# Performance work log

Measured on AMD Instinct MI355X. Metric: run time of the kernel, lower is better.

The kernel has to match this reference:

```python
import jax, jax.numpy as jnp
import numpy as np

VOCAB = 50257
EMB = 1024
HID = 1024
B, T = 8, 256


def setup_inputs() -> dict:
    key = jax.random.key(0)
    ks = jax.random.split(key, 6)
    s = 0.05  # small init scale for numerical sanity
    return {
        "x": jax.random.randint(ks[0], (B, T), 0, VOCAB, dtype=jnp.int64) if jax.config.jax_enable_x64 else jax.random.randint(ks[0], (B, T), 0, VOCAB, dtype=jnp.int32),
        "emb_W": jax.random.normal(ks[1], (VOCAB, EMB), dtype=jnp.float32) * s,
        "W_ih": jax.random.normal(ks[2], (4 * HID, EMB), dtype=jnp.float32) * s,
        "W_hh": jax.random.normal(ks[3], (4 * HID, HID), dtype=jnp.float32) * s,
        "b_ih": jax.random.normal(ks[4], (4 * HID,), dtype=jnp.float32) * s,
        "b_hh": jax.random.normal(ks[5], (4 * HID,), dtype=jnp.float32) * s,
        "dec_b": jnp.zeros((VOCAB,), dtype=jnp.float32),
    }


def _lstm(emb, W_ih, W_hh, b_ih, b_hh):
    # emb: [B, T, E]. Precompute input projections for all timesteps (one big GEMM).
    x_proj = jnp.einsum("bte,ge->btg", emb, W_ih) + (b_ih + b_hh)  # [B, T, 4H]
    h0 = jnp.zeros((emb.shape[0], HID), emb.dtype)
    c0 = jnp.zeros((emb.shape[0], HID), emb.dtype)

    def step(carry, xt):  # xt: [B, 4H]
        h, c = carry
        g = xt + h @ W_hh.T  # [B, 4H]
        i, f, gg, o = jnp.split(g, 4, axis=-1)  # PyTorch gate order i,f,g,o
        i = jax.nn.sigmoid(i)
        f = jax.nn.sigmoid(f)
        gg = jnp.tanh(gg)
        o = jax.nn.sigmoid(o)
        c_new = f * c + i * gg
        h_new = o * jnp.tanh(c_new)
        return (h_new, c_new), h_new

    (hT, cT), hs = jax.lax.scan(step, (h0, c0), jnp.swapaxes(x_proj, 0, 1))
    out = jnp.swapaxes(hs, 0, 1)  # [B, T, H], batch_first
    return out, (hT[None], cT[None])  # num_layers=1 leading dim


def reference(x, emb_W, W_ih, W_hh, b_ih, b_hh, dec_b):
    emb = emb_W[x]                                   # [B, T, E]
    out, hidden = _lstm(emb, W_ih, W_hh, b_ih, b_hh)  # [B, T, H]
    logits = jnp.einsum("bth,vh->btv", out, emb_W) + dec_b  # tied decoder
    logits = logits.reshape(-1, VOCAB)
    return jax.nn.log_softmax(logits, axis=1), hidden
```

## Files before the change

kernel.cpp:

```cpp
#include <hip/hip_runtime.h>

typedef float f32x4 __attribute__((ext_vector_type(4)));
typedef __bf16 bf16x8 __attribute__((ext_vector_type(8)));
typedef unsigned int u32x4 __attribute__((ext_vector_type(4)));
typedef unsigned short u16;
typedef unsigned int u32;

#define VOCAB 50257
#define KDIM 1024
#define MROWS 2048
#define TSEQ 256
#define NBLK 64
#define NHELP 192
#define NTILE 393
#define NT (NTILE * 2)
#define LOGN ((size_t)MROWS * VOCAB)

__device__ __forceinline__ u16 f2bf(float f) {
    u32 u = __builtin_bit_cast(u32, f);
    u = (u + 0x7FFFu + ((u >> 16) & 1u)) >> 16;
    return (u16)u;
}

__device__ __forceinline__ float sigm(float x) { return 1.0f / (1.0f + __expf(-x)); }

__device__ __forceinline__ u32 min4u(u32x4 v) {
    u32 a = v.x < v.y ? v.x : v.y;
    u32 b = v.z < v.w ? v.z : v.w;
    return a < b ? a : b;
}


__global__ void conv_bf16(const float4* __restrict__ in, ushort4* __restrict__ out, long n4) {
    long i = (long)blockIdx.x * blockDim.x + threadIdx.x;
    long stride = (long)gridDim.x * blockDim.x;
    for (; i < n4; i += stride) {
        float4 v = in[i];
        ushort4 o;
        o.x = f2bf(v.x); o.y = f2bf(v.y); o.z = f2bf(v.z); o.w = f2bf(v.w);
        out[i] = o;
    }
}

__global__ void bias_sum(const float* __restrict__ a, const float* __restrict__ b,
                         float* __restrict__ o) {
    int i = blockIdx.x * 256 + threadIdx.x;
    if (i < 4096) o[i] = a[i] + b[i];
}

__global__ __launch_bounds__(256) void gather_emb(const int* __restrict__ x,
                                                  const float* __restrict__ embW,
                                                  u16* __restrict__ out) {
    int m = blockIdx.x;
    int row = x[m];
    const float4* src = (const float4*)(embW + (size_t)row * KDIM);
    ushort4* dst = (ushort4*)(out + (size_t)m * KDIM);
    float4 v = src[threadIdx.x];
    ushort4 o;
    o.x = f2bf(v.x); o.y = f2bf(v.y); o.z = f2bf(v.z); o.w = f2bf(v.w);
    dst[threadIdx.x] = o;
}

__global__ void init_hseq(u32* __restrict__ hs) {
    int i = blockIdx.x * 256 + threadIdx.x;
    if (i < 257 * 4096) hs[i] = (i < 4096) ? 0x00010001u : 0u;
}


#define BM 128
#define BN 128
#define BK 64

__device__ __forceinline__ void gl_lds16(const u16* g, const u16* l) {
    __builtin_amdgcn_global_load_lds(
        (const __attribute__((address_space(1))) u32*)g,
        (__attribute__((address_space(3))) u32*)l, 16, 0, 0);
}

__global__ __launch_bounds__(256, 2)
void gemm_bt(const u16* __restrict__ A, const u16* __restrict__ Bm,
             const float* __restrict__ bias, float* __restrict__ C,
             int N, int Nb, int K, int ldc)
{
    __shared__ __align__(16) u16 As[BM * BK];
    __shared__ __align__(16) u16 Bs[BN * BK];
    const int tid  = threadIdx.x;
    const int lane = tid & 63;
    const int wid  = tid >> 6;

    const int gx  = gridDim.x;
    const int nwg = gx * gridDim.y;
    const int lin = blockIdx.y * gx + blockIdx.x;
    const int qq = nwg >> 3, rr = nwg & 7;
    const int xcd = lin & 7, idx = lin >> 3;
    const int neu = (xcd < rr) ? (xcd * (qq + 1) + idx)
                               : (rr * (qq + 1) + (xcd - rr) * qq + idx);
    const int bm = neu % gx;
    const int bn = neu / gx;

    const int wr = wid >> 1, wc = wid & 1;

    const u16* gA[4]; const u16* gB[4];
    const u16* ldsA[4]; const u16* ldsB[4];
#pragma unroll
    for (int r = 0; r < 4; ++r) {
        int L = r * 256 + tid;
        int row = L >> 3, ps = L & 7;
        int ls = ps ^ (row & 7);
        gA[r] = A + (size_t)(bm * BM + row) * K + ls * 8;
        int brow = bn * BN + row; brow = brow < Nb ? brow : Nb - 1;
        gB[r] = Bm + (size_t)brow * K + ls * 8;
        ldsA[r] = As + (r * 256 + wid * 64) * 8;
        ldsB[r] = Bs + (r * 256 + wid * 64) * 8;
    }

    const int lrow = lane & 15, ksl = lane >> 4;
    int aoff[4][2], boff[4][2];
#pragma unroll
    for (int i = 0; i < 4; ++i)
#pragma unroll
        for (int ks = 0; ks < 2; ++ks) {
            int ar = wr * 64 + i * 16 + lrow;
            aoff[i][ks] = ar * BK + (((ks * 4 + ksl) ^ (ar & 7)) * 8);
            int br = wc * 64 + i * 16 + lrow;
            boff[i][ks] = br * BK + (((ks * 4 + ksl) ^ (br & 7)) * 8);
        }

    f32x4 acc[4][4] = {};
    for (int kt = 0; kt < K; kt += BK) {
#pragma unroll
        for (int r = 0; r < 4; ++r) gl_lds16(gA[r] + kt, ldsA[r]);
#pragma unroll
        for (int r = 0; r < 4; ++r) gl_lds16(gB[r] + kt, ldsB[r]);
        __syncthreads();
        bf16x8 af[4][2], bfb[4][2];
#pragma unroll
        for (int i = 0; i < 4; ++i)
#pragma unroll
            for (int ks = 0; ks < 2; ++ks) {
                af[i][ks]  = *(const bf16x8*)(As + aoff[i][ks]);
                bfb[i][ks] = *(const bf16x8*)(Bs + boff[i][ks]);
            }
#pragma unroll
        for (int ks = 0; ks < 2; ++ks)
#pragma unroll
            for (int mi = 0; mi < 4; ++mi)
#pragma unroll
                for (int ni = 0; ni < 4; ++ni)
                    acc[mi][ni] = __builtin_amdgcn_mfma_f32_16x16x32_bf16(
                        af[mi][ks], bfb[ni][ks], acc[mi][ni], 0, 0, 0);
        __syncthreads();
    }

    const int crl = lane >> 4, ccl = lane & 15;
    const int row0 = bm * BM + wr * 64, col0 = bn * BN + wc * 64;
#pragma unroll
    for (int ni = 0; ni < 4; ++ni) {
        int col = col0 + ni * 16 + ccl;
        if (col < N) {
            float bv = bias[col];
#pragma unroll
            for (int mi = 0; mi < 4; ++mi) {
                int row = row0 + mi * 16 + crl * 4;
                float* cp = C + (size_t)row * ldc + col;
#pragma unroll
                for (int r = 0; r < 4; ++r)
                    cp[(size_t)r * ldc] = acc[mi][ni][r] + bv;
            }
        }
    }
}


__global__ __launch_bounds__(256, 2)
void gemm_dec(const u16* __restrict__ A, const u16* __restrict__ Bm,
              const float* __restrict__ bias, u16* __restrict__ Cb,
              float* __restrict__ pmax, float* __restrict__ psum)
{
    const int N = VOCAB, Nb = VOCAB, K = KDIM;
    __shared__ __align__(16) u16 As[BM * BK];
    __shared__ __align__(16) u16 Bs[BN * BK];
    const int tid  = threadIdx.x;
    const int lane = tid & 63;
    const int wid  = tid >> 6;

    const int gx  = gridDim.x;
    const int nwg = gx * gridDim.y;
    const int lin = blockIdx.y * gx + blockIdx.x;
    const int qq = nwg >> 3, rr = nwg & 7;
    const int xcd = lin & 7, idx = lin >> 3;
    const int neu = (xcd < rr) ? (xcd * (qq + 1) + idx)
                               : (rr * (qq + 1) + (xcd - rr) * qq + idx);
    const int bm = neu % gx;
    const int bn = neu / gx;

    const int wr = wid >> 1, wc = wid & 1;

    const u16* gA[4]; const u16* gB[4];
    const u16* ldsA[4]; const u16* ldsB[4];
#pragma unroll
    for (int r = 0; r < 4; ++r) {
        int L = r * 256 + tid;
        int row = L >> 3, ps = L & 7;
        int ls = ps ^ (row & 7);
        gA[r] = A + (size_t)(bm * BM + row) * K + ls * 8;
        int brow = bn * BN + row; brow = brow < Nb ? brow : Nb - 1;
        gB[r] = Bm + (size_t)brow * K + ls * 8;
        ldsA[r] = As + (r * 256 + wid * 64) * 8;
        ldsB[r] = Bs + (r * 256 + wid * 64) * 8;
    }

    const int lrow = lane & 15, ksl = lane >> 4;
    int aoff[4][2], boff[4][2];
#pragma unroll
    for (int i = 0; i < 4; ++i)
#pragma unroll
        for (int ks = 0; ks < 2; ++ks) {
            int ar = wr * 64 + i * 16 + lrow;
            aoff[i][ks] = ar * BK + (((ks * 4 + ksl) ^ (ar & 7)) * 8);
            int br = wc * 64 + i * 16 + lrow;
            boff[i][ks] = br * BK + (((ks * 4 + ksl) ^ (br & 7)) * 8);
        }

    f32x4 acc[4][4] = {};
    for (int kt = 0; kt < K; kt += BK) {
#pragma unroll
        for (int r = 0; r < 4; ++r) gl_lds16(gA[r] + kt, ldsA[r]);
#pragma unroll
        for (int r = 0; r < 4; ++r) gl_lds16(gB[r] + kt, ldsB[r]);
        __syncthreads();
        bf16x8 af[4][2], bfb[4][2];
#pragma unroll
        for (int i = 0; i < 4; ++i)
#pragma unroll
            for (int ks = 0; ks < 2; ++ks) {
                af[i][ks]  = *(const bf16x8*)(As + aoff[i][ks]);
                bfb[i][ks] = *(const bf16x8*)(Bs + boff[i][ks]);
            }
#pragma unroll
        for (int ks = 0; ks < 2; ++ks)
#pragma unroll
            for (int mi = 0; mi < 4; ++mi)
#pragma unroll
                for (int ni = 0; ni < 4; ++ni)
                    acc[mi][ni] = __builtin_amdgcn_mfma_f32_16x16x32_bf16(
                        af[mi][ks], bfb[ni][ks], acc[mi][ni], 0, 0, 0);
        __syncthreads();
    }

    const int crl = lane >> 4, ccl = lane & 15;
    const int row0 = bm * BM + wr * 64, col0 = bn * BN + wc * 64;
    float bve[4]; bool vld[4];
#pragma unroll
    for (int ni = 0; ni < 4; ++ni) {
        int col = col0 + ni * 16 + ccl;
        vld[ni] = col < N;
        bve[ni] = vld[ni] ? bias[col] : 0.f;
    }
#pragma unroll
    for (int ni = 0; ni < 4; ++ni) {
        if (vld[ni]) {
            int col = col0 + ni * 16 + ccl;
#pragma unroll
            for (int mi = 0; mi < 4; ++mi) {
                int row = row0 + mi * 16 + crl * 4;
                u16* cp = Cb + (size_t)row * (VOCAB * 2) + col;
#pragma unroll
                for (int r = 0; r < 4; ++r)
                    cp[(size_t)r * (VOCAB * 2)] = f2bf(acc[mi][ni][r] + bve[ni]);
            }
        }
    }
#pragma unroll
    for (int mi = 0; mi < 4; ++mi)
#pragma unroll
        for (int r = 0; r < 4; ++r) {
            int row = row0 + mi * 16 + crl * 4 + r;
            float v0 = vld[0] ? acc[mi][0][r] + bve[0] : -3.0e38f;
            float v1 = vld[1] ? acc[mi][1][r] + bve[1] : -3.0e38f;
            float v2 = vld[2] ? acc[mi][2][r] + bve[2] : -3.0e38f;
            float v3 = vld[3] ? acc[mi][3][r] + bve[3] : -3.0e38f;
            float rmax = fmaxf(fmaxf(v0, v1), fmaxf(v2, v3));
#pragma unroll
            for (int m2 = 1; m2 < 16; m2 <<= 1) rmax = fmaxf(rmax, __shfl_xor(rmax, m2));
            float rs = __expf(v0 - rmax) + __expf(v1 - rmax) +
                       __expf(v2 - rmax) + __expf(v3 - rmax);
#pragma unroll
            for (int m2 = 1; m2 < 16; m2 <<= 1) rs += __shfl_xor(rs, m2);
            if (ccl == 0) {
                pmax[(size_t)row * NT + bn * 2 + wc] = rmax;
                psum[(size_t)row * NT + bn * 2 + wc] = rs;
            }
        }
}


__global__ __launch_bounds__(256, 1)
void lstm_persist(const u16* __restrict__ Whh,
                  const float* __restrict__ xproj,
                  u16* __restrict__ hseq,
                  u16* __restrict__ hall,
                  float* __restrict__ outTail,
                  const float4* __restrict__ embW,
                  ushort4* __restrict__ embW_bf)
{
    const int tid = threadIdx.x;
    const int bid = blockIdx.x;

    if (bid >= NBLK) {
        long i = (long)(bid - NBLK) * 256 + tid;
        const long n4 = (long)VOCAB * KDIM / 4;
        const long stride = (long)NHELP * 256;
        for (; i < n4; i += stride) {
            float4 v = embW[i];
            ushort4 o;
            o.x = f2bf(v.x); o.y = f2bf(v.y); o.z = f2bf(v.z); o.w = f2bf(v.w);
            embW_bf[i] = o;
        }
        return;
    }

    const int lane = tid & 63;
    const int wq   = tid >> 6;
    const int lrow = lane & 15, ksl = lane >> 4;
    const int colbase = bid * 16;

    bf16x8 Bf[32];
    {
        const u16* bp = Whh + (size_t)(wq * 1024 + colbase + lrow) * KDIM + ksl * 8;
#pragma unroll
        for (int kk = 0; kk < 32; ++kk)
            asm volatile("global_load_dwordx4 %0, %1, off"
                         : "=v"(Bf[kk]) : "v"(bp + kk * 32));
        asm volatile("s_waitcnt vmcnt(0)" ::: "memory");
        __builtin_amdgcn_sched_barrier(0);
    }

    __shared__ float S[4][8][16];
    __shared__ __align__(16) u16 hstage[2][16384];

    for (int i = tid; i < 2 * 64 * 8; i += 256) {
        int buf = i >> 9, rem = i & 511;
        int j = rem >> 3, rowoff = rem & 7;
        u32x4 z = {0, 0, 0, 0};
        *(u32x4*)(&hstage[buf][j * 256 + 128 + rowoff * 16]) = z;
        *(u32x4*)(&hstage[buf][j * 256 + 128 + rowoff * 16 + 8]) = z;
    }

    const bool upd = tid < 128;
    const int b8 = tid >> 4, c16 = tid & 15;
    float creg = 0.f;
    float xp0 = 0.f, xp1 = 0.f, xp2 = 0.f, xp3 = 0.f;
    size_t xbase = 0;
    if (upd) {
        xbase = (size_t)b8 * TSEQ * 4096 + colbase + c16;
        xp0 = xproj[xbase];          xp1 = xproj[xbase + 1024];
        xp2 = xproj[xbase + 2048];   xp3 = xproj[xbase + 3072];
    }

    const int pj = tid >> 2, pr = (tid & 3) * 2;
    const int sw = (pj & 7) << 3;
    int widx[4];
#pragma unroll
    for (int k = 0; k < 4; ++k)
        widx[k] = pj * 256 + ((pr * 16 + k * 8) ^ sw);

    int aro[4];
#pragma unroll
    for (int i = 0; i < 4; ++i) {
        int swr = ((2 * i + (ksl >> 1)) & 7) << 3;
        aro[i] = (ksl >> 1) * 256 + ((lrow * 16 + (ksl & 1) * 8) ^ swr);
    }

    for (int t = 0; t < TSEQ; ++t) {
        const u32* src = (const u32*)hseq + (size_t)t * 4096 + pj * 64 + pr * 8;
        u32x4 P0, P1, P2, P3;
        for (;;) {
            asm volatile("global_load_dwordx4 %0, %1, off sc0 sc1" : "=v"(P0) : "v"(src));
            asm volatile("global_load_dwordx4 %0, %1, off sc0 sc1" : "=v"(P1) : "v"(src + 4));
            asm volatile("global_load_dwordx4 %0, %1, off sc0 sc1" : "=v"(P2) : "v"(src + 8));
            asm volatile("global_load_dwordx4 %0, %1, off sc0 sc1" : "=v"(P3) : "v"(src + 12));
            asm volatile("s_waitcnt vmcnt(0)" ::: "memory");
            __builtin_amdgcn_sched_barrier(0);
            u32 a = min4u(P0), b = min4u(P1), c = min4u(P2), d = min4u(P3);
            u32 mn = (a < b ? a : b); u32 mn2 = (c < d ? c : d);
            if ((mn < mn2 ? mn : mn2) != 0u) break;
        }
        {
            u16* hb = &hstage[t & 1][0];
            *(u32x4*)(hb + widx[0]) = P0;
            *(u32x4*)(hb + widx[1]) = P1;
            *(u32x4*)(hb + widx[2]) = P2;
            *(u32x4*)(hb + widx[3]) = P3;
        }
        __syncthreads();

        const u16* sb = &hstage[t & 1][0];
        f32x4 ac0 = {}, ac1 = {}, ac2 = {}, ac3 = {};
#pragma unroll
        for (int g = 0; g < 8; ++g) {
            bf16x8 a0 = *(const bf16x8*)(sb + g * 2048 + 0 * 512 + aro[0]);
            bf16x8 a1 = *(const bf16x8*)(sb + g * 2048 + 1 * 512 + aro[1]);
            bf16x8 a2 = *(const bf16x8*)(sb + g * 2048 + 2 * 512 + aro[2]);
            bf16x8 a3 = *(const bf16x8*)(sb + g * 2048 + 3 * 512 + aro[3]);
            ac0 = __builtin_amdgcn_mfma_f32_16x16x32_bf16(a0, Bf[g * 4 + 0], ac0, 0, 0, 0);
            ac1 = __builtin_amdgcn_mfma_f32_16x16x32_bf16(a1, Bf[g * 4 + 1], ac1, 0, 0, 0);
            ac2 = __builtin_amdgcn_mfma_f32_16x16x32_bf16(a2, Bf[g * 4 + 2], ac2, 0, 0, 0);
            ac3 = __builtin_amdgcn_mfma_f32_16x16x32_bf16(a3, Bf[g * 4 + 3], ac3, 0, 0, 0);
        }
        if (ksl < 2) {
#pragma unroll
            for (int r = 0; r < 4; ++r)
                S[wq][ksl * 4 + r][lrow] = ac0[r] + ac1[r] + ac2[r] + ac3[r];
        }
        __syncthreads();

        if (upd) {
            float gi = S[0][b8][c16] + xp0;
            float gf = S[1][b8][c16] + xp1;
            float gg = S[2][b8][c16] + xp2;
            float go = S[3][b8][c16] + xp3;
            float iv = sigm(gi), fv = sigm(gf), ov = sigm(go);
            float gv = tanhf(gg);
            creg = fv * creg + iv * gv;
            float hv = ov * tanhf(creg);
            u16 hbx = f2bf(hv) | 1;
            int w0 = (int)hbx;
            int w1 = __shfl_down(w0, 1);
            if (!(c16 & 1)) {
                u32 w = (u32)(u16)w0 | ((u32)(u16)w1 << 16);
                u32* dst = (u32*)hseq + (size_t)(t + 1) * 4096 + bid * 64 + b8 * 8 + (c16 >> 1);
                __hip_atomic_store(dst, w, __ATOMIC_RELAXED, __HIP_MEMORY_SCOPE_AGENT);
            }
            hall[((size_t)b8 * TSEQ + t) * KDIM + colbase + c16] = hbx;
            if (t == TSEQ - 1) {
                outTail[b8 * KDIM + colbase + c16] = hv;
                outTail[8192 + b8 * KDIM + colbase + c16] = creg;
            }
            int tn = (t + 1 < TSEQ) ? t + 1 : t;
            size_t xb = xbase + (size_t)tn * 4096;
            xp0 = xproj[xb];        xp1 = xproj[xb + 1024];
            xp2 = xproj[xb + 2048]; xp3 = xproj[xb + 3072];
        }
    }
}


__global__ __launch_bounds__(256)
void merge_lse(const float* __restrict__ pmax, const float* __restrict__ psum,
               float* __restrict__ lse) {
    const int m = blockIdx.x;
    const int tid = threadIdx.x;
    __shared__ float smx[4], ssm[4];
    float mx = -3.0e38f, s = 0.f;
    for (int i = tid; i < NT; i += 256) {
        float pm = pmax[(size_t)m * NT + i];
        float ps = psum[(size_t)m * NT + i];
        if (pm > mx) { s *= __expf(mx - pm); mx = pm; }
        s += ps * __expf(pm - mx);
    }
#pragma unroll
    for (int off = 32; off > 0; off >>= 1) {
        float om = __shfl_xor(mx, off), os = __shfl_xor(s, off);
        float nm = fmaxf(mx, om);
        s = s * __expf(mx - nm) + os * __expf(om - nm);
        mx = nm;
    }
    if ((tid & 63) == 0) { smx[tid >> 6] = mx; ssm[tid >> 6] = s; }
    __syncthreads();
    if (tid == 0) {
        float M = fmaxf(fmaxf(smx[0], smx[1]), fmaxf(smx[2], smx[3]));
        float S4 = ssm[0] * __expf(smx[0] - M) + ssm[1] * __expf(smx[1] - M) +
                   ssm[2] * __expf(smx[2] - M) + ssm[3] * __expf(smx[3] - M);
        lse[m] = M + __logf(S4);
    }
}

__global__ __launch_bounds__(256)
void final_sub(float* __restrict__ out, const float* __restrict__ lse) {
    const int m = blockIdx.x;
    const float L = lse[m];
    const u32* srcw = (const u32*)out + (size_t)m * VOCAB;
    float* dst = out + (size_t)m * VOCAB;
    const int tid = threadIdx.x;
    const int NCH = (VOCAB + 2047) / 2048;
    for (int c = NCH - 1; c >= 0; --c) {
        int e0 = c * 2048 + tid * 8;
        int w0i = e0 >> 1;
        u32 w0 = srcw[w0i], w1 = srcw[w0i + 1], w2 = srcw[w0i + 2], w3 = srcw[w0i + 3];
        __syncthreads();
        float f[8];
        f[0] = __builtin_bit_cast(float, (w0 & 0xFFFFu) << 16) - L;
        f[1] = __builtin_bit_cast(float, w0 & 0xFFFF0000u) - L;
        f[2] = __builtin_bit_cast(float, (w1 & 0xFFFFu) << 16) - L;
        f[3] = __builtin_bit_cast(float, w1 & 0xFFFF0000u) - L;
        f[4] = __builtin_bit_cast(float, (w2 & 0xFFFFu) << 16) - L;
        f[5] = __builtin_bit_cast(float, w2 & 0xFFFF0000u) - L;
        f[6] = __builtin_bit_cast(float, (w3 & 0xFFFFu) << 16) - L;
        f[7] = __builtin_bit_cast(float, w3 & 0xFFFF0000u) - L;
        if (e0 + 8 <= VOCAB) {
#pragma unroll
            for (int k = 0; k < 8; ++k) dst[e0 + k] = f[k];
        } else {
#pragma unroll
            for (int k = 0; k < 8; ++k) if (e0 + k < VOCAB) dst[e0 + k] = f[k];
        }
    }
}


extern "C" void kernel_launch(void* const* d_in, const int* in_sizes, int n_in,
                              void* d_out, int out_size, void* d_ws, size_t ws_size,
                              hipStream_t stream)
{
    const int*   x    = (const int*)d_in[0];
    const float* embW = (const float*)d_in[1];
    const float* Wih  = (const float*)d_in[2];
    const float* Whh  = (const float*)d_in[3];
    const float* bih  = (const float*)d_in[4];
    const float* bhh  = (const float*)d_in[5];
    const float* decb = (const float*)d_in[6];
    float* out = (float*)d_out;

    char* p = (char*)d_ws;
    auto carve = [&](size_t bytes) {
        char* q = p;
        p += (bytes + 255) & ~(size_t)255;
        return q;
    };
    u16*   embW_bf = (u16*)carve((size_t)VOCAB * KDIM * 2);
    u16*   Wih_bf  = (u16*)carve((size_t)4096 * KDIM * 2);
    u16*   Whh_bf  = (u16*)carve((size_t)4096 * KDIM * 2);
    u16*   emb_bf  = (u16*)carve((size_t)MROWS * KDIM * 2);
    float* xproj   = (float*)carve((size_t)MROWS * 4096 * 4);
    u16*   hall_bf = (u16*)carve((size_t)MROWS * KDIM * 2);
    u16*   hseq    = (u16*)carve((size_t)(TSEQ + 1) * 4096 * 4);
    float* pmax    = (float*)carve((size_t)MROWS * NT * 4);
    float* psum    = (float*)carve((size_t)MROWS * NT * 4);
    float* lse     = (float*)carve((size_t)MROWS * 4);
    float* bsum    = (float*)carve((size_t)4096 * 4);

    init_hseq<<<(257 * 4096 + 255) / 256, 256, 0, stream>>>((u32*)hseq);

    conv_bf16<<<1024, 256, 0, stream>>>((const float4*)Wih, (ushort4*)Wih_bf,
                                        (long)4096 * KDIM / 4);
    conv_bf16<<<1024, 256, 0, stream>>>((const float4*)Whh, (ushort4*)Whh_bf,
                                        (long)4096 * KDIM / 4);
    bias_sum<<<16, 256, 0, stream>>>(bih, bhh, bsum);
    gather_emb<<<MROWS, 256, 0, stream>>>(x, embW, emb_bf);

    {
        dim3 g(MROWS / BM, 4096 / BN);
        gemm_bt<<<g, 256, 0, stream>>>(emb_bf, Wih_bf, bsum, xproj, 4096, 4096, KDIM, 4096);
    }

    lstm_persist<<<NBLK + NHELP, 256, 0, stream>>>(Whh_bf, xproj, hseq, hall_bf,
                                                   out + LOGN,
                                                   (const float4*)embW,
                                                   (ushort4*)embW_bf);

    {
        dim3 g(MROWS / BM, NTILE);
        gemm_dec<<<g, 256, 0, stream>>>(hall_bf, embW_bf, decb, (u16*)out, pmax, psum);
    }

    merge_lse<<<MROWS, 256, 0, stream>>>(pmax, psum, lse);
    final_sub<<<MROWS, 256, 0, stream>>>(out, lse);
}
```

Baseline: 1.217 ms.

## Place persistent LSTM blocks on one XCD and use cheaper coherent polling

Each block reads its XCD id and takes a per-XCD ticket. The first XCD to collect 64 blocks becomes the leader, and only its blocks run the recurrent LSTM, so the per-step h exchange stays inside one die's L2. Every other block converts the embedding table to bf16. Polling first uses L2-coherent (sc0) loads and falls back to system-coherent loads after 8 tries. Each h store is written twice, once to the local L2 and once system-coherent. The launch becomes cooperative with 512 blocks at 2 blocks per CU to guarantee co-residency. The cost is extra atomics and memsets, and it relies on the hardware mapping blocks to XCDs.

```diff
diff --git a/kernel.cpp b/kernel.cpp
--- a/kernel.cpp
+++ b/kernel.cpp
@@ -11,7 +11,7 @@
 #define MROWS 2048
 #define TSEQ 256
 #define NBLK 64
-#define NHELP 192
+#define NTOT 512
 #define NTILE 393
 #define NT (NTILE * 2)
 #define LOGN ((size_t)MROWS * VOCAB)
@@ -295,22 +295,54 @@
 }
 
 
-__global__ __launch_bounds__(256, 1)
+__global__ __launch_bounds__(256, 2)
 void lstm_persist(const u16* __restrict__ Whh,
                   const float* __restrict__ xproj,
                   u16* __restrict__ hseq,
                   u16* __restrict__ hall,
                   float* __restrict__ outTail,
                   const float4* __restrict__ embW,
-                  ushort4* __restrict__ embW_bf)
+                  ushort4* __restrict__ embW_bf,
+                  u32* __restrict__ cnt,
+                  u32* __restrict__ leader,
+                  u32* __restrict__ helpc)
 {
     const int tid = threadIdx.x;
-    const int bid = blockIdx.x;
-
-    if (bid >= NBLK) {
-        long i = (long)(bid - NBLK) * 256 + tid;
+    __shared__ u32 roleS;
+
+    if (tid == 0) {
+        u32 xcd;
+        asm volatile("s_getreg_b32 %0, hwreg(HW_REG_XCC_ID)" : "=s"(xcd));
+        xcd &= 7u;
+        u32 ticket = __hip_atomic_fetch_add(&cnt[xcd * 32], 1u,
+                                            __ATOMIC_RELAXED, __HIP_MEMORY_SCOPE_AGENT);
+        u32 slot = 0xFFFFFFFFu;
+        if (ticket < NBLK) {
+            if (ticket == NBLK - 1) {
+                u32 expect = 0xFFFFFFFFu;
+                __hip_atomic_compare_exchange_strong(leader, &expect, xcd,
+                    __ATOMIC_RELAXED, __ATOMIC_RELAXED, __HIP_MEMORY_SCOPE_AGENT);
+            }
+            u32 L;
+            while ((L = __hip_atomic_load(leader, __ATOMIC_RELAXED,
+                                          __HIP_MEMORY_SCOPE_AGENT)) == 0xFFFFFFFFu)
+                __builtin_amdgcn_s_sleep(2);
+            if (L == xcd) slot = ticket;
+        }
+        roleS = slot;
+    }
+    __syncthreads();
+    const u32 slot = roleS;
+
+    if (slot == 0xFFFFFFFFu) {
+        __shared__ u32 hidxS;
+        if (tid == 0)
+            hidxS = __hip_atomic_fetch_add(helpc, 1u,
+                                           __ATOMIC_RELAXED, __HIP_MEMORY_SCOPE_AGENT);
+        __syncthreads();
+        long i = (long)hidxS * 256 + tid;
         const long n4 = (long)VOCAB * KDIM / 4;
-        const long stride = (long)NHELP * 256;
+        const long stride = (long)(NTOT - NBLK) * 256;
         for (; i < n4; i += stride) {
             float4 v = embW[i];
             ushort4 o;
@@ -323,7 +355,7 @@
     const int lane = tid & 63;
     const int wq   = tid >> 6;
     const int lrow = lane & 15, ksl = lane >> 4;
-    const int colbase = bid * 16;
+    const int colbase = slot * 16;
 
     bf16x8 Bf[32];
     {
@@ -375,11 +407,18 @@
     for (int t = 0; t < TSEQ; ++t) {
         const u32* src = (const u32*)hseq + (size_t)t * 4096 + pj * 64 + pr * 8;
         u32x4 P0, P1, P2, P3;
-        for (;;) {
-            asm volatile("global_load_dwordx4 %0, %1, off sc0 sc1" : "=v"(P0) : "v"(src));
-            asm volatile("global_load_dwordx4 %0, %1, off sc0 sc1" : "=v"(P1) : "v"(src + 4));
-            asm volatile("global_load_dwordx4 %0, %1, off sc0 sc1" : "=v"(P2) : "v"(src + 8));
-            asm volatile("global_load_dwordx4 %0, %1, off sc0 sc1" : "=v"(P3) : "v"(src + 12));
+        for (int tries = 0;; ++tries) {
+            if (tries < 8) {
+                asm volatile("global_load_dwordx4 %0, %1, off sc0" : "=v"(P0) : "v"(src));
+                asm volatile("global_load_dwordx4 %0, %1, off sc0" : "=v"(P1) : "v"(src + 4));
+                asm volatile("global_load_dwordx4 %0, %1, off sc0" : "=v"(P2) : "v"(src + 8));
+                asm volatile("global_load_dwordx4 %0, %1, off sc0" : "=v"(P3) : "v"(src + 12));
+            } else {
+                asm volatile("global_load_dwordx4 %0, %1, off sc0 sc1" : "=v"(P0) : "v"(src));
+                asm volatile("global_load_dwordx4 %0, %1, off sc0 sc1" : "=v"(P1) : "v"(src + 4));
+                asm volatile("global_load_dwordx4 %0, %1, off sc0 sc1" : "=v"(P2) : "v"(src + 8));
+                asm volatile("global_load_dwordx4 %0, %1, off sc0 sc1" : "=v"(P3) : "v"(src + 12));
+            }
             asm volatile("s_waitcnt vmcnt(0)" ::: "memory");
             __builtin_amdgcn_sched_barrier(0);
             u32 a = min4u(P0), b = min4u(P1), c = min4u(P2), d = min4u(P3);
@@ -429,8 +468,10 @@
             int w1 = __shfl_down(w0, 1);
             if (!(c16 & 1)) {
                 u32 w = (u32)(u16)w0 | ((u32)(u16)w1 << 16);
-                u32* dst = (u32*)hseq + (size_t)(t + 1) * 4096 + bid * 64 + b8 * 8 + (c16 >> 1);
-                __hip_atomic_store(dst, w, __ATOMIC_RELAXED, __HIP_MEMORY_SCOPE_AGENT);
+                u32* dst = (u32*)hseq + (size_t)(t + 1) * 4096 + slot * 64 + b8 * 8 + (c16 >> 1);
+                asm volatile("global_store_dword %0, %1, off\n\t"
+                             "global_store_dword %0, %1, off sc0 sc1"
+                             :: "v"(dst), "v"(w) : "memory");
             }
             hall[((size_t)b8 * TSEQ + t) * KDIM + colbase + c16] = hbx;
             if (t == TSEQ - 1) {
@@ -539,6 +580,13 @@
     float* psum    = (float*)carve((size_t)MROWS * NT * 4);
     float* lse     = (float*)carve((size_t)MROWS * 4);
     float* bsum    = (float*)carve((size_t)4096 * 4);
+    u32*   cnt     = (u32*)carve(8 * 32 * 4);
+    u32*   leader  = (u32*)carve(256);
+    u32*   helpc   = (u32*)carve(256);
+
+    hipMemsetAsync(cnt, 0, 8 * 32 * 4, stream);
+    hipMemsetAsync(leader, 0xFF, 4, stream);
+    hipMemsetAsync(helpc, 0, 4, stream);
 
     init_hseq<<<(257 * 4096 + 255) / 256, 256, 0, stream>>>((u32*)hseq);
 
@@ -554,10 +602,21 @@
         gemm_bt<<<g, 256, 0, stream>>>(emb_bf, Wih_bf, bsum, xproj, 4096, 4096, KDIM, 4096);
     }
 
-    lstm_persist<<<NBLK + NHELP, 256, 0, stream>>>(Whh_bf, xproj, hseq, hall_bf,
-                                                   out + LOGN,
-                                                   (const float4*)embW,
-                                                   (ushort4*)embW_bf);
+    {
+        const u16* a0 = Whh_bf; const float* a1 = xproj; u16* a2 = hseq;
+        u16* a3 = hall_bf; float* a4 = out + LOGN;
+        const float4* a5 = (const float4*)embW; ushort4* a6 = (ushort4*)embW_bf;
+        u32* a7 = cnt; u32* a8 = leader; u32* a9 = helpc;
+        void* args[] = { &a0, &a1, &a2, &a3, &a4, &a5, &a6, &a7, &a8, &a9 };
+        hipError_t e = hipLaunchCooperativeKernel((const void*)lstm_persist,
+                                                  dim3(NTOT), dim3(256),
+                                                  args, 0, stream);
+        if (e != hipSuccess) {
+            lstm_persist<<<NTOT, 256, 0, stream>>>(Whh_bf, xproj, hseq, hall_bf,
+                                                   out + LOGN, (const float4*)embW,
+                                                   (ushort4*)embW_bf, cnt, leader, helpc);
+        }
+    }
 
     {
         dim3 g(MROWS / BM, NTILE);
```

New measurement: 2.041 ms. 67.8% more time.

## Interleave W_hh gate rows so LSTM cell update runs in-register without LDS barrier

Applied to the files above, without the earlier changes.

Reorders the W_hh rows loaded per lane so each MFMA output quad holds the i,f,g,o gates of one hidden column. Gates are then gathered with lane shuffles and the cell update is done directly in registers, removing the shared-memory gate buffer and one __syncthreads per timestep on the serial recurrent critical path. The trade-off is that fewer lanes (a quarter of those in the first half of each wave) do the nonlinearities, each handling four batch rows, and the per-step xproj loads become more scattered.

```diff
diff --git a/kernel.cpp b/kernel.cpp
--- a/kernel.cpp
+++ b/kernel.cpp
@@ -321,13 +321,15 @@
     }
 
     const int lane = tid & 63;
-    const int wq   = tid >> 6;
+    const int w    = tid >> 6;
     const int lrow = lane & 15, ksl = lane >> 4;
     const int colbase = bid * 16;
+    const int q  = lrow & 3;
+    const int cc = lrow >> 2;
 
     bf16x8 Bf[32];
     {
-        const u16* bp = Whh + (size_t)(wq * 1024 + colbase + lrow) * KDIM + ksl * 8;
+        const u16* bp = Whh + (size_t)(q * 1024 + colbase + w * 4 + cc) * KDIM + ksl * 8;
 #pragma unroll
         for (int kk = 0; kk < 32; ++kk)
             asm volatile("global_load_dwordx4 %0, %1, off"
@@ -336,7 +338,6 @@
         __builtin_amdgcn_sched_barrier(0);
     }
 
-    __shared__ float S[4][8][16];
     __shared__ __align__(16) u16 hstage[2][16384];
 
     for (int i = tid; i < 2 * 64 * 8; i += 256) {
@@ -347,15 +348,17 @@
         *(u32x4*)(&hstage[buf][j * 256 + 128 + rowoff * 16 + 8]) = z;
     }
 
-    const bool upd = tid < 128;
-    const int b8 = tid >> 4, c16 = tid & 15;
-    float creg = 0.f;
-    float xp0 = 0.f, xp1 = 0.f, xp2 = 0.f, xp3 = 0.f;
-    size_t xbase = 0;
-    if (upd) {
-        xbase = (size_t)b8 * TSEQ * 4096 + colbase + c16;
-        xp0 = xproj[xbase];          xp1 = xproj[xbase + 1024];
-        xp2 = xproj[xbase + 2048];   xp3 = xproj[xbase + 3072];
+    const int mycol = colbase + w * 4 + cc;
+    const bool updl = (q == 0) && (ksl < 2);
+    f32x4 creg = {};
+    f32x4 xg0 = {}, xg1 = {}, xg2 = {}, xg3 = {};
+    if (updl) {
+#pragma unroll
+        for (int r = 0; r < 4; ++r) {
+            size_t xb = ((size_t)(ksl * 4 + r) * TSEQ) * 4096 + mycol;
+            xg0[r] = xproj[xb];        xg1[r] = xproj[xb + 1024];
+            xg2[r] = xproj[xb + 2048]; xg3[r] = xproj[xb + 3072];
+        }
     }
 
     const int pj = tid >> 2, pr = (tid & 3) * 2;
@@ -387,11 +390,11 @@
             if ((mn < mn2 ? mn : mn2) != 0u) break;
         }
         {
-            u16* hb = &hstage[t & 1][0];
-            *(u32x4*)(hb + widx[0]) = P0;
-            *(u32x4*)(hb + widx[1]) = P1;
-            *(u32x4*)(hb + widx[2]) = P2;
-            *(u32x4*)(hb + widx[3]) = P3;
+            u16* hb2 = &hstage[t & 1][0];
+            *(u32x4*)(hb2 + widx[0]) = P0;
+            *(u32x4*)(hb2 + widx[1]) = P1;
+            *(u32x4*)(hb2 + widx[2]) = P2;
+            *(u32x4*)(hb2 + widx[3]) = P3;
         }
         __syncthreads();
 
@@ -408,39 +411,65 @@
             ac2 = __builtin_amdgcn_mfma_f32_16x16x32_bf16(a2, Bf[g * 4 + 2], ac2, 0, 0, 0);
             ac3 = __builtin_amdgcn_mfma_f32_16x16x32_bf16(a3, Bf[g * 4 + 3], ac3, 0, 0, 0);
         }
-        if (ksl < 2) {
-#pragma unroll
-            for (int r = 0; r < 4; ++r)
-                S[wq][ksl * 4 + r][lrow] = ac0[r] + ac1[r] + ac2[r] + ac3[r];
-        }
-        __syncthreads();
-
-        if (upd) {
-            float gi = S[0][b8][c16] + xp0;
-            float gf = S[1][b8][c16] + xp1;
-            float gg = S[2][b8][c16] + xp2;
-            float go = S[3][b8][c16] + xp3;
-            float iv = sigm(gi), fv = sigm(gf), ov = sigm(go);
-            float gv = tanhf(gg);
-            creg = fv * creg + iv * gv;
-            float hv = ov * tanhf(creg);
-            u16 hbx = f2bf(hv) | 1;
-            int w0 = (int)hbx;
-            int w1 = __shfl_down(w0, 1);
-            if (!(c16 & 1)) {
-                u32 w = (u32)(u16)w0 | ((u32)(u16)w1 << 16);
-                u32* dst = (u32*)hseq + (size_t)(t + 1) * 4096 + bid * 64 + b8 * 8 + (c16 >> 1);
-                __hip_atomic_store(dst, w, __ATOMIC_RELAXED, __HIP_MEMORY_SCOPE_AGENT);
-            }
-            hall[((size_t)b8 * TSEQ + t) * KDIM + colbase + c16] = hbx;
+
+        f32x4 D = ac0 + ac1 + ac2 + ac3;
+        float s1x[4], s2x[4], s3x[4];
+#pragma unroll
+        for (int r = 0; r < 4; ++r) {
+            s1x[r] = __shfl_down(D[r], 1);
+            s2x[r] = __shfl_down(D[r], 2);
+            s3x[r] = __shfl_down(D[r], 3);
+        }
+
+        float hv[4] = {0.f, 0.f, 0.f, 0.f};
+        int hb[4] = {0, 0, 0, 0};
+        if (updl) {
+#pragma unroll
+            for (int r = 0; r < 4; ++r) {
+                float gi = D[r]   + xg0[r];
+                float gf = s1x[r] + xg1[r];
+                float gg = s2x[r] + xg2[r];
+                float go = s3x[r] + xg3[r];
+                float iv = sigm(gi), fv = sigm(gf), ov = sigm(go);
+                float gv = tanhf(gg);
+                creg[r] = fv * creg[r] + iv * gv;
+                hv[r] = ov * tanhf(creg[r]);
+                hb[r] = (int)(f2bf(hv[r]) | 1);
+            }
+        }
+        int nb0 = __shfl_down(hb[0], 4);
+        int nb1 = __shfl_down(hb[1], 4);
+        int nb2 = __shfl_down(hb[2], 4);
+        int nb3 = __shfl_down(hb[3], 4);
+
+        if (updl) {
+            if (!(cc & 1)) {
+                int nbv[4] = {nb0, nb1, nb2, nb3};
+#pragma unroll
+                for (int r = 0; r < 4; ++r) {
+                    u32 wp = (u32)(u16)hb[r] | ((u32)(u16)nbv[r] << 16);
+                    u32* dst = (u32*)hseq + (size_t)(t + 1) * 4096 + bid * 64
+                               + (ksl * 4 + r) * 8 + ((w * 4 + cc) >> 1);
+                    __hip_atomic_store(dst, wp, __ATOMIC_RELAXED, __HIP_MEMORY_SCOPE_AGENT);
+                    u32* hd = (u32*)hall
+                              + (((size_t)(ksl * 4 + r) * TSEQ + t) * KDIM + mycol) / 2;
+                    *hd = wp;
+                }
+            }
             if (t == TSEQ - 1) {
-                outTail[b8 * KDIM + colbase + c16] = hv;
-                outTail[8192 + b8 * KDIM + colbase + c16] = creg;
+#pragma unroll
+                for (int r = 0; r < 4; ++r) {
+                    outTail[(ksl * 4 + r) * KDIM + mycol] = hv[r];
+                    outTail[8192 + (ksl * 4 + r) * KDIM + mycol] = creg[r];
+                }
             }
             int tn = (t + 1 < TSEQ) ? t + 1 : t;
-            size_t xb = xbase + (size_t)tn * 4096;
-            xp0 = xproj[xb];        xp1 = xproj[xb + 1024];
-            xp2 = xproj[xb + 2048]; xp3 = xproj[xb + 3072];
+#pragma unroll
+            for (int r = 0; r < 4; ++r) {
+                size_t xb = ((size_t)(ksl * 4 + r) * TSEQ + tn) * 4096 + mycol;
+                xg0[r] = xproj[xb];        xg1[r] = xproj[xb + 1024];
+                xg2[r] = xproj[xb + 2048]; xg3[r] = xproj[xb + 3072];
+            }
         }
     }
 }
```

Result: slower. 1.887 ms (+55.1%).

## Fuse decoder GEMM into persistent LSTM kernel with dynamic tile queue

Applied to the files above, without the earlier changes.

Removes the separate decoder GEMM launch. Helper blocks, after converting the embedding to bf16, and the LSTM blocks, after finishing the recurrence, pull decoder tiles from an atomic work queue. Each tile spin-waits until its 128 rows of hidden states are flagged ready in hall, so decoding overlaps the serial recurrence. The cost is that the 64 recurrence blocks share the GPU with concurrent GEMM work, which may slow the latency-critical LSTM chain. It also adds polling, coherent loads of the A operand through registers instead of direct-to-LDS loads, and only 256 resident blocks with one block per CU.

```diff
diff --git a/kernel.cpp b/kernel.cpp
--- a/kernel.cpp
+++ b/kernel.cpp
@@ -3,6 +3,7 @@
 typedef float f32x4 __attribute__((ext_vector_type(4)));
 typedef __bf16 bf16x8 __attribute__((ext_vector_type(8)));
 typedef unsigned int u32x4 __attribute__((ext_vector_type(4)));
+typedef unsigned int u32x2 __attribute__((ext_vector_type(2)));
 typedef unsigned short u16;
 typedef unsigned int u32;
 
@@ -14,6 +15,7 @@
 #define NHELP 192
 #define NTILE 393
 #define NT (NTILE * 2)
+#define NTILES_TOT (16 * NTILE)
 #define LOGN ((size_t)MROWS * VOCAB)
 
 __device__ __forceinline__ u16 f2bf(float f) {
@@ -66,6 +68,11 @@
     if (i < 257 * 4096) hs[i] = (i < 4096) ? 0x00010001u : 0u;
 }
 
+__global__ void zero_hall(u32* __restrict__ h) {
+    int i = blockIdx.x * 256 + threadIdx.x;
+    if (i < MROWS * (KDIM / 2)) h[i] = 0u;
+}
+
 
 #define BM 128
 #define BN 128
@@ -172,45 +179,29 @@
 }
 
 
-__global__ __launch_bounds__(256, 2)
-void gemm_dec(const u16* __restrict__ A, const u16* __restrict__ Bm,
-              const float* __restrict__ bias, u16* __restrict__ Cb,
-              float* __restrict__ pmax, float* __restrict__ psum)
+__device__ __forceinline__ void dec_tile(
+    const u16* __restrict__ A, const u16* __restrict__ Bm,
+    const float* __restrict__ bias, u16* __restrict__ Cb,
+    float* __restrict__ pmax, float* __restrict__ psum,
+    u16* As, u16* Bs, int bm, int bn, int tid)
 {
-    const int N = VOCAB, Nb = VOCAB, K = KDIM;
-    __shared__ __align__(16) u16 As[BM * BK];
-    __shared__ __align__(16) u16 Bs[BN * BK];
-    const int tid  = threadIdx.x;
     const int lane = tid & 63;
     const int wid  = tid >> 6;
-
-    const int gx  = gridDim.x;
-    const int nwg = gx * gridDim.y;
-    const int lin = blockIdx.y * gx + blockIdx.x;
-    const int qq = nwg >> 3, rr = nwg & 7;
-    const int xcd = lin & 7, idx = lin >> 3;
-    const int neu = (xcd < rr) ? (xcd * (qq + 1) + idx)
-                               : (rr * (qq + 1) + (xcd - rr) * qq + idx);
-    const int bm = neu % gx;
-    const int bn = neu / gx;
-
     const int wr = wid >> 1, wc = wid & 1;
-
-    const u16* gA[4]; const u16* gB[4];
-    const u16* ldsA[4]; const u16* ldsB[4];
+    const int lrow = lane & 15, ksl = lane >> 4;
+
+    const u16* gB[4]; const u16* ldsB[4];
+    const u16* gA[4]; u16* wA[4];
 #pragma unroll
     for (int r = 0; r < 4; ++r) {
         int L = r * 256 + tid;
         int row = L >> 3, ps = L & 7;
-        int ls = ps ^ (row & 7);
-        gA[r] = A + (size_t)(bm * BM + row) * K + ls * 8;
-        int brow = bn * BN + row; brow = brow < Nb ? brow : Nb - 1;
-        gB[r] = Bm + (size_t)brow * K + ls * 8;
-        ldsA[r] = As + (r * 256 + wid * 64) * 8;
+        int brow = bn * BN + row; brow = brow < VOCAB ? brow : VOCAB - 1;
+        gB[r] = Bm + (size_t)brow * KDIM + (ps ^ (row & 7)) * 8;
         ldsB[r] = Bs + (r * 256 + wid * 64) * 8;
-    }
-
-    const int lrow = lane & 15, ksl = lane >> 4;
+        gA[r] = A + (size_t)(bm * BM + row) * KDIM + ps * 8;
+        wA[r] = As + row * BK + ((ps ^ (row & 7)) * 8);
+    }
     int aoff[4][2], boff[4][2];
 #pragma unroll
     for (int i = 0; i < 4; ++i)
@@ -223,11 +214,18 @@
         }
 
     f32x4 acc[4][4] = {};
-    for (int kt = 0; kt < K; kt += BK) {
-#pragma unroll
-        for (int r = 0; r < 4; ++r) gl_lds16(gA[r] + kt, ldsA[r]);
+    for (int kt = 0; kt < KDIM; kt += BK) {
+        bf16x8 Ar[4];
 #pragma unroll
         for (int r = 0; r < 4; ++r) gl_lds16(gB[r] + kt, ldsB[r]);
+#pragma unroll
+        for (int r = 0; r < 4; ++r)
+            asm volatile("global_load_dwordx4 %0, %1, off sc0 sc1"
+                         : "=v"(Ar[r]) : "v"(gA[r] + kt));
+        asm volatile("s_waitcnt vmcnt(0)" ::: "memory");
+        __builtin_amdgcn_sched_barrier(0);
+#pragma unroll
+        for (int r = 0; r < 4; ++r) *(bf16x8*)wA[r] = Ar[r];
         __syncthreads();
         bf16x8 af[4][2], bfb[4][2];
 #pragma unroll
@@ -254,7 +252,7 @@
 #pragma unroll
     for (int ni = 0; ni < 4; ++ni) {
         int col = col0 + ni * 16 + ccl;
-        vld[ni] = col < N;
+        vld[ni] = col < VOCAB;
         bve[ni] = vld[ni] ? bias[col] : 0.f;
     }
 #pragma unroll
@@ -302,10 +300,19 @@
                   u16* __restrict__ hall,
                   float* __restrict__ outTail,
                   const float4* __restrict__ embW,
-                  ushort4* __restrict__ embW_bf)
+                  u16* __restrict__ embW_bf,
+                  const float* __restrict__ decb,
+                  u16* __restrict__ Cb,
+                  float* __restrict__ pmax, float* __restrict__ psum,
+                  u32* __restrict__ qcnt,
+                  u32* __restrict__ convc)
 {
     const int tid = threadIdx.x;
     const int bid = blockIdx.x;
+
+    __shared__ float S[4][8][16];
+    __shared__ __align__(16) u16 hstage[2][16384];
+    __shared__ int tileS;
 
     if (bid >= NBLK) {
         long i = (long)(bid - NBLK) * 256 + tid;
@@ -315,133 +322,172 @@
             float4 v = embW[i];
             ushort4 o;
             o.x = f2bf(v.x); o.y = f2bf(v.y); o.z = f2bf(v.z); o.w = f2bf(v.w);
-            embW_bf[i] = o;
-        }
-        return;
-    }
-
-    const int lane = tid & 63;
-    const int wq   = tid >> 6;
-    const int lrow = lane & 15, ksl = lane >> 4;
-    const int colbase = bid * 16;
-
-    bf16x8 Bf[32];
-    {
-        const u16* bp = Whh + (size_t)(wq * 1024 + colbase + lrow) * KDIM + ksl * 8;
-#pragma unroll
-        for (int kk = 0; kk < 32; ++kk)
-            asm volatile("global_load_dwordx4 %0, %1, off"
-                         : "=v"(Bf[kk]) : "v"(bp + kk * 32));
+            asm volatile("global_store_dwordx2 %0, %1, off sc0 sc1"
+                         :: "v"((ushort4*)embW_bf + i), "v"(o) : "memory");
+        }
         asm volatile("s_waitcnt vmcnt(0)" ::: "memory");
-        __builtin_amdgcn_sched_barrier(0);
-    }
-
-    __shared__ float S[4][8][16];
-    __shared__ __align__(16) u16 hstage[2][16384];
-
-    for (int i = tid; i < 2 * 64 * 8; i += 256) {
-        int buf = i >> 9, rem = i & 511;
-        int j = rem >> 3, rowoff = rem & 7;
-        u32x4 z = {0, 0, 0, 0};
-        *(u32x4*)(&hstage[buf][j * 256 + 128 + rowoff * 16]) = z;
-        *(u32x4*)(&hstage[buf][j * 256 + 128 + rowoff * 16 + 8]) = z;
-    }
-
-    const bool upd = tid < 128;
-    const int b8 = tid >> 4, c16 = tid & 15;
-    float creg = 0.f;
-    float xp0 = 0.f, xp1 = 0.f, xp2 = 0.f, xp3 = 0.f;
-    size_t xbase = 0;
-    if (upd) {
-        xbase = (size_t)b8 * TSEQ * 4096 + colbase + c16;
-        xp0 = xproj[xbase];          xp1 = xproj[xbase + 1024];
-        xp2 = xproj[xbase + 2048];   xp3 = xproj[xbase + 3072];
-    }
-
-    const int pj = tid >> 2, pr = (tid & 3) * 2;
-    const int sw = (pj & 7) << 3;
-    int widx[4];
-#pragma unroll
-    for (int k = 0; k < 4; ++k)
-        widx[k] = pj * 256 + ((pr * 16 + k * 8) ^ sw);
-
-    int aro[4];
-#pragma unroll
-    for (int i = 0; i < 4; ++i) {
-        int swr = ((2 * i + (ksl >> 1)) & 7) << 3;
-        aro[i] = (ksl >> 1) * 256 + ((lrow * 16 + (ksl & 1) * 8) ^ swr);
-    }
-
-    for (int t = 0; t < TSEQ; ++t) {
-        const u32* src = (const u32*)hseq + (size_t)t * 4096 + pj * 64 + pr * 8;
-        u32x4 P0, P1, P2, P3;
-        for (;;) {
-            asm volatile("global_load_dwordx4 %0, %1, off sc0 sc1" : "=v"(P0) : "v"(src));
-            asm volatile("global_load_dwordx4 %0, %1, off sc0 sc1" : "=v"(P1) : "v"(src + 4));
-            asm volatile("global_load_dwordx4 %0, %1, off sc0 sc1" : "=v"(P2) : "v"(src + 8));
-            asm volatile("global_load_dwordx4 %0, %1, off sc0 sc1" : "=v"(P3) : "v"(src + 12));
+        if (tid == 0) {
+            __hip_atomic_fetch_add(convc, 1u, __ATOMIC_RELAXED, __HIP_MEMORY_SCOPE_AGENT);
+            while (__hip_atomic_load(convc, __ATOMIC_RELAXED,
+                                     __HIP_MEMORY_SCOPE_AGENT) < (u32)NHELP)
+                __builtin_amdgcn_s_sleep(4);
+        }
+        __syncthreads();
+    } else {
+        const int lane = tid & 63;
+        const int wq   = tid >> 6;
+        const int lrow = lane & 15, ksl = lane >> 4;
+        const int colbase = bid * 16;
+
+        bf16x8 Bf[32];
+        {
+            const u16* bp = Whh + (size_t)(wq * 1024 + colbase + lrow) * KDIM + ksl * 8;
+#pragma unroll
+            for (int kk = 0; kk < 32; ++kk)
+                asm volatile("global_load_dwordx4 %0, %1, off"
+                             : "=v"(Bf[kk]) : "v"(bp + kk * 32));
             asm volatile("s_waitcnt vmcnt(0)" ::: "memory");
             __builtin_amdgcn_sched_barrier(0);
-            u32 a = min4u(P0), b = min4u(P1), c = min4u(P2), d = min4u(P3);
-            u32 mn = (a < b ? a : b); u32 mn2 = (c < d ? c : d);
-            if ((mn < mn2 ? mn : mn2) != 0u) break;
-        }
-        {
-            u16* hb = &hstage[t & 1][0];
-            *(u32x4*)(hb + widx[0]) = P0;
-            *(u32x4*)(hb + widx[1]) = P1;
-            *(u32x4*)(hb + widx[2]) = P2;
-            *(u32x4*)(hb + widx[3]) = P3;
-        }
-        __syncthreads();
-
-        const u16* sb = &hstage[t & 1][0];
-        f32x4 ac0 = {}, ac1 = {}, ac2 = {}, ac3 = {};
-#pragma unroll
-        for (int g = 0; g < 8; ++g) {
-            bf16x8 a0 = *(const bf16x8*)(sb + g * 2048 + 0 * 512 + aro[0]);
-            bf16x8 a1 = *(const bf16x8*)(sb + g * 2048 + 1 * 512 + aro[1]);
-            bf16x8 a2 = *(const bf16x8*)(sb + g * 2048 + 2 * 512 + aro[2]);
-            bf16x8 a3 = *(const bf16x8*)(sb + g * 2048 + 3 * 512 + aro[3]);
-            ac0 = __builtin_amdgcn_mfma_f32_16x16x32_bf16(a0, Bf[g * 4 + 0], ac0, 0, 0, 0);
-            ac1 = __builtin_amdgcn_mfma_f32_16x16x32_bf16(a1, Bf[g * 4 + 1], ac1, 0, 0, 0);
-            ac2 = __builtin_amdgcn_mfma_f32_16x16x32_bf16(a2, Bf[g * 4 + 2], ac2, 0, 0, 0);
-            ac3 = __builtin_amdgcn_mfma_f32_16x16x32_bf16(a3, Bf[g * 4 + 3], ac3, 0, 0, 0);
-        }
-        if (ksl < 2) {
-#pragma unroll
-            for (int r = 0; r < 4; ++r)
-                S[wq][ksl * 4 + r][lrow] = ac0[r] + ac1[r] + ac2[r] + ac3[r];
-        }
-        __syncthreads();
-
+        }
+
+        for (int i = tid; i < 2 * 64 * 8; i += 256) {
+            int buf = i >> 9, rem = i & 511;
+            int j = rem >> 3, rowoff = rem & 7;
+            u32x4 z = {0, 0, 0, 0};
+            *(u32x4*)(&hstage[buf][j * 256 + 128 + rowoff * 16]) = z;
+            *(u32x4*)(&hstage[buf][j * 256 + 128 + rowoff * 16 + 8]) = z;
+        }
+
+        const bool upd = tid < 128;
+        const int b8 = tid >> 4, c16 = tid & 15;
+        float creg = 0.f;
+        float xp0 = 0.f, xp1 = 0.f, xp2 = 0.f, xp3 = 0.f;
+        size_t xbase = 0;
         if (upd) {
-            float gi = S[0][b8][c16] + xp0;
-            float gf = S[1][b8][c16] + xp1;
-            float gg = S[2][b8][c16] + xp2;
-            float go = S[3][b8][c16] + xp3;
-            float iv = sigm(gi), fv = sigm(gf), ov = sigm(go);
-            float gv = tanhf(gg);
-            creg = fv * creg + iv * gv;
-            float hv = ov * tanhf(creg);
-            u16 hbx = f2bf(hv) | 1;
-            int w0 = (int)hbx;
-            int w1 = __shfl_down(w0, 1);
-            if (!(c16 & 1)) {
-                u32 w = (u32)(u16)w0 | ((u32)(u16)w1 << 16);
-                u32* dst = (u32*)hseq + (size_t)(t + 1) * 4096 + bid * 64 + b8 * 8 + (c16 >> 1);
-                __hip_atomic_store(dst, w, __ATOMIC_RELAXED, __HIP_MEMORY_SCOPE_AGENT);
-            }
-            hall[((size_t)b8 * TSEQ + t) * KDIM + colbase + c16] = hbx;
-            if (t == TSEQ - 1) {
-                outTail[b8 * KDIM + colbase + c16] = hv;
-                outTail[8192 + b8 * KDIM + colbase + c16] = creg;
-            }
-            int tn = (t + 1 < TSEQ) ? t + 1 : t;
-            size_t xb = xbase + (size_t)tn * 4096;
-            xp0 = xproj[xb];        xp1 = xproj[xb + 1024];
-            xp2 = xproj[xb + 2048]; xp3 = xproj[xb + 3072];
-        }
+            xbase = (size_t)b8 * TSEQ * 4096 + colbase + c16;
+            xp0 = xproj[xbase];          xp1 = xproj[xbase + 1024];
+            xp2 = xproj[xbase + 2048];   xp3 = xproj[xbase + 3072];
+        }
+
+        const int pj = tid >> 2, pr = (tid & 3) * 2;
+        const int sw = (pj & 7) << 3;
+        int widx[4];
+#pragma unroll
+        for (int k = 0; k < 4; ++k)
+            widx[k] = pj * 256 + ((pr * 16 + k * 8) ^ sw);
+
+        int aro[4];
+#pragma unroll
+        for (int i = 0; i < 4; ++i) {
+            int swr = ((2 * i + (ksl >> 1)) & 7) << 3;
+            aro[i] = (ksl >> 1) * 256 + ((lrow * 16 + (ksl & 1) * 8) ^ swr);
+        }
+
+        for (int t = 0; t < TSEQ; ++t) {
+            const u32* src = (const u32*)hseq + (size_t)t * 4096 + pj * 64 + pr * 8;
+            u32x4 P0, P1, P2, P3;
+            for (;;) {
+                asm volatile("global_load_dwordx4 %0, %1, off sc0 sc1" : "=v"(P0) : "v"(src));
+                asm volatile("global_load_dwordx4 %0, %1, off sc0 sc1" : "=v"(P1) : "v"(src + 4));
+                asm volatile("global_load_dwordx4 %0, %1, off sc0 sc1" : "=v"(P2) : "v"(src + 8));
+                asm volatile("global_load_dwordx4 %0, %1, off sc0 sc1" : "=v"(P3) : "v"(src + 12));
+                asm volatile("s_waitcnt vmcnt(0)" ::: "memory");
+                __builtin_amdgcn_sched_barrier(0);
+                u32 a = min4u(P0), b = min4u(P1), c = min4u(P2), d = min4u(P3);
+                u32 mn = (a < b ? a : b); u32 mn2 = (c < d ? c : d);
+                if ((mn < mn2 ? mn : mn2) != 0u) break;
+            }
+            {
+                u16* hb2 = &hstage[t & 1][0];
+                *(u32x4*)(hb2 + widx[0]) = P0;
+                *(u32x4*)(hb2 + widx[1]) = P1;
+                *(u32x4*)(hb2 + widx[2]) = P2;
+                *(u32x4*)(hb2 + widx[3]) = P3;
+            }
+            __syncthreads();
+
+            const u16* sb = &hstage[t & 1][0];
+            f32x4 ac0 = {}, ac1 = {}, ac2 = {}, ac3 = {};
+#pragma unroll
+            for (int g = 0; g < 8; ++g) {
+                bf16x8 a0 = *(const bf16x8*)(sb + g * 2048 + 0 * 512 + aro[0]);
+                bf16x8 a1 = *(const bf16x8*)(sb + g * 2048 + 1 * 512 + aro[1]);
+                bf16x8 a2 = *(const bf16x8*)(sb + g * 2048 + 2 * 512 + aro[2]);
+                bf16x8 a3 = *(const bf16x8*)(sb + g * 2048 + 3 * 512 + aro[3]);
+                ac0 = __builtin_amdgcn_mfma_f32_16x16x32_bf16(a0, Bf[g * 4 + 0], ac0, 0, 0, 0);
+                ac1 = __builtin_amdgcn_mfma_f32_16x16x32_bf16(a1, Bf[g * 4 + 1], ac1, 0, 0, 0);
+                ac2 = __builtin_amdgcn_mfma_f32_16x16x32_bf16(a2, Bf[g * 4 + 2], ac2, 0, 0, 0);
+                ac3 = __builtin_amdgcn_mfma_f32_16x16x32_bf16(a3, Bf[g * 4 + 3], ac3, 0, 0, 0);
+            }
+            if (ksl < 2) {
+#pragma unroll
+                for (int r = 0; r < 4; ++r)
+                    S[wq][ksl * 4 + r][lrow] = ac0[r] + ac1[r] + ac2[r] + ac3[r];
+            }
+            __syncthreads();
+
+            if (upd) {
+                float gi = S[0][b8][c16] + xp0;
+                float gf = S[1][b8][c16] + xp1;
+                float gg = S[2][b8][c16] + xp2;
+                float go = S[3][b8][c16] + xp3;
+                float iv = sigm(gi), fv = sigm(gf), ov = sigm(go);
+                float gv = tanhf(gg);
+                creg = fv * creg + iv * gv;
+                float hv = ov * tanhf(creg);
+                u16 hbx = f2bf(hv) | 1;
+                int w0 = (int)hbx;
+                int w1 = __shfl_down(w0, 1);
+                if (!(c16 & 1)) {
+                    u32 wp = (u32)(u16)w0 | ((u32)(u16)w1 << 16);
+                    u32* dst = (u32*)hseq + (size_t)(t + 1) * 4096 + bid * 64
+                               + b8 * 8 + (c16 >> 1);
+                    __hip_atomic_store(dst, wp, __ATOMIC_RELAXED, __HIP_MEMORY_SCOPE_AGENT);
+                    u32* hd = (u32*)hall
+                              + ((((size_t)b8 * TSEQ + t) * KDIM + colbase + c16) >> 1);
+                    __hip_atomic_store(hd, wp, __ATOMIC_RELAXED, __HIP_MEMORY_SCOPE_AGENT);
+                }
+                if (t == TSEQ - 1) {
+                    outTail[b8 * KDIM + colbase + c16] = hv;
+                    outTail[8192 + b8 * KDIM + colbase + c16] = creg;
+                }
+                int tn = (t + 1 < TSEQ) ? t + 1 : t;
+                size_t xb = xbase + (size_t)tn * 4096;
+                xp0 = xproj[xb];        xp1 = xproj[xb + 1024];
+                xp2 = xproj[xb + 2048]; xp3 = xproj[xb + 3072];
+            }
+        }
+        if (tid == 0) {
+            while (__hip_atomic_load(convc, __ATOMIC_RELAXED,
+                                     __HIP_MEMORY_SCOPE_AGENT) < (u32)NHELP)
+                __builtin_amdgcn_s_sleep(4);
+        }
+        __syncthreads();
+    }
+
+    u16* As = &hstage[0][0];
+    u16* Bs = &hstage[0][8192];
+    for (;;) {
+        if (tid == 0)
+            tileS = (int)__hip_atomic_fetch_add(qcnt, 1u,
+                                                __ATOMIC_RELAXED, __HIP_MEMORY_SCOPE_AGENT);
+        __syncthreads();
+        int tileid = tileS;
+        if (tileid >= NTILES_TOT) break;
+        int bm = tileid & 15, bn = tileid >> 4;
+
+        const u32* rp = (const u32*)hall + (size_t)(bm * BM + 127) * (KDIM / 2) + tid * 2;
+        for (;;) {
+            u32x2 v;
+            asm volatile("global_load_dwordx2 %0, %1, off sc0 sc1" : "=v"(v) : "v"(rp));
+            asm volatile("s_waitcnt vmcnt(0)" ::: "memory");
+            int ok = ((v.x & 0x00010001u) == 0x00010001u) &&
+                     ((v.y & 0x00010001u) == 0x00010001u);
+            if (__syncthreads_and(ok)) break;
+            __builtin_amdgcn_s_sleep(8);
+        }
+        dec_tile(hall, embW_bf, decb, Cb, pmax, psum, As, Bs, bm, bn, tid);
+        __syncthreads();
     }
 }
 
@@ -539,8 +585,14 @@
     float* psum    = (float*)carve((size_t)MROWS * NT * 4);
     float* lse     = (float*)carve((size_t)MROWS * 4);
     float* bsum    = (float*)carve((size_t)4096 * 4);
+    u32*   qcnt    = (u32*)carve(256);
+    u32*   convc   = (u32*)carve(256);
+
+    hipMemsetAsync(qcnt, 0, 4, stream);
+    hipMemsetAsync(convc, 0, 4, stream);
 
     init_hseq<<<(257 * 4096 + 255) / 256, 256, 0, stream>>>((u32*)hseq);
+    zero_hall<<<(MROWS * (KDIM / 2) + 255) / 256, 256, 0, stream>>>((u32*)hall_bf);
 
     conv_bf16<<<1024, 256, 0, stream>>>((const float4*)Wih, (ushort4*)Wih_bf,
                                         (long)4096 * KDIM / 4);
@@ -556,13 +608,9 @@
 
     lstm_persist<<<NBLK + NHELP, 256, 0, stream>>>(Whh_bf, xproj, hseq, hall_bf,
                                                    out + LOGN,
-                                                   (const float4*)embW,
-                                                   (ushort4*)embW_bf);
-
-    {
-        dim3 g(MROWS / BM, NTILE);
-        gemm_dec<<<g, 256, 0, stream>>>(hall_bf, embW_bf, decb, (u16*)out, pmax, psum);
-    }
+                                                   (const float4*)embW, embW_bf,
+                                                   decb, (u16*)out, pmax, psum,
+                                                   qcnt, convc);
 
     merge_lse<<<MROWS, 256, 0, stream>>>(pmax, psum, lse);
     final_sub<<<MROWS, 256, 0, stream>>>(out, lse);
```

New measurement: 1.616 ms. 1.33x slower.
